# Optimization experiments

Measured on AMD Instinct MI355X. Metric: run time of the kernel, lower is better.

Reference implementation:

```python
import jax, jax.numpy as jnp
import numpy as np

T, H, I, E = 1024, 2048, 3200, 8  # tokens, hidden, intermediate, experts
JITTER_EPS = 0.01


def sparsemixer(scores, jitter_eps=JITTER_EPS):
    # ---- top-1 ----
    max1 = jnp.max(scores, axis=-1, keepdims=True)
    ind1 = jnp.argmax(scores, axis=-1, keepdims=True)  # first-max, matches torch
    factor = jnp.maximum(jnp.abs(scores), max1)        # clamp(min=max1)
    mask = (max1 - scores) / factor > 2.0 * jitter_eps
    masked_gates = jax.nn.softmax(jnp.where(mask, -jnp.inf, scores), axis=-1)
    mult1 = jnp.take_along_axis(masked_gates, ind1, axis=-1)
    # ---- mask out top-1, then top-2 ----
    top1_onehot = jax.nn.one_hot(ind1[..., 0], scores.shape[-1], dtype=bool)
    masked_scores = jnp.where(top1_onehot, -jnp.inf, scores)
    max2 = jnp.max(masked_scores, axis=-1, keepdims=True)
    ind2 = jnp.argmax(masked_scores, axis=-1, keepdims=True)
    factor2 = jnp.maximum(jnp.abs(scores), max2)
    mask2 = (max2 - scores) / factor2 > 2.0 * jitter_eps
    masked_gates2 = jax.nn.softmax(jnp.where(mask2, -jnp.inf, masked_scores), axis=-1)
    mult2 = jnp.take_along_axis(masked_gates2, ind2, axis=-1)
    multiplier = jnp.concatenate([mult1, mult2], axis=-1)       # [T, 2]
    selected = jnp.concatenate([ind1, ind2], axis=-1)           # [T, 2] int
    return multiplier, selected


def setup_inputs() -> dict:
    key = jax.random.key(0)
    k0, k1, k2, k3, k4 = jax.random.split(key, 5)
    hidden_states = jax.random.normal(k0, (T, H), dtype=jnp.float32)
    gate_w = jax.random.normal(k1, (E, H), dtype=jnp.float32) * (H ** -0.5)
    w1 = jax.random.normal(k2, (E, I, H), dtype=jnp.float32) * (H ** -0.5)
    w3 = jax.random.normal(k3, (E, I, H), dtype=jnp.float32) * (H ** -0.5)
    w2 = jax.random.normal(k4, (E, H, I), dtype=jnp.float32) * (I ** -0.5)
    return {"hidden_states": hidden_states, "gate_w": gate_w,
            "w1": w1, "w3": w3, "w2": w2}


def reference(hidden_states, gate_w, w1, w3, w2):
    x = hidden_states.reshape(-1, gate_w.shape[1])              # [T, H]
    router_logits = x @ gate_w.T                                # [T, E]
    topk_w, topk_ids = sparsemixer(router_logits)               # [T,2], [T,2]
    n_exp = gate_w.shape[0]
    # combine top-2 (weight, id) pairs into a dense [T, E] gate matrix
    gates = jnp.sum(jax.nn.one_hot(topk_ids, n_exp, dtype=x.dtype)
                    * topk_w[..., None], axis=1)                # [T, E]
    # SiLU-gated expert MLPs, combined with routing gates
    h1 = jnp.einsum('th,eih->tei', x, w1)                       # [T, E, I]
    h3 = jnp.einsum('th,eih->tei', x, w3)
    act = jax.nn.silu(h1) * h3                                  # [T, E, I]
    out = jnp.einsum('tei,ehi,te->th', act, w2, gates)          # [T, H]
    return out.reshape(hidden_states.shape)
```

## Files before the change

kernel.cpp:

```cpp
#include <hip/hip_runtime.h>

#define T_ 1024
#define H_ 2048
#define I_ 3200
#define E_ 8

typedef float fvec4 __attribute__((ext_vector_type(4)));
typedef float f32x4 __attribute__((ext_vector_type(4)));
typedef __bf16 bf16x8 __attribute__((ext_vector_type(8)));
typedef unsigned short u16x4 __attribute__((ext_vector_type(4)));

typedef const __attribute__((address_space(1))) void* gp1_t;
typedef __attribute__((address_space(3))) void* sp3_t;

#define WS_CHUNK 128
#define WS_TOK   512
#define WS_GATE  33280
#define WS_XB    66560
#define WS_ACT   4261888
#define MAXCH    20

#define BARX() { asm volatile("s_waitcnt lgkmcnt(0)" ::: "memory"); \
    __builtin_amdgcn_sched_barrier(0); __builtin_amdgcn_s_barrier(); \
    __builtin_amdgcn_sched_barrier(0); }

__global__ __launch_bounds__(256) void router_kernel(const float* __restrict__ x,
                                                     const float* __restrict__ gw,
                                                     int* __restrict__ cnt,
                                                     int* __restrict__ tok,
                                                     float* __restrict__ gate,
                                                     unsigned short* __restrict__ xb) {
  const int lane = threadIdx.x & 63;
  const int wv = threadIdx.x >> 6;
  const int t = blockIdx.x * 4 + wv;

  const float* xp = x + (size_t)t * H_;
  fvec4 xr[8];
#pragma unroll
  for (int j = 0; j < 8; ++j) xr[j] = *(const fvec4*)(xp + j * 256 + lane * 4);

  unsigned short* xbp = xb + (size_t)t * H_;
#pragma unroll
  for (int j = 0; j < 8; ++j) {
    u16x4 o;
#pragma unroll
    for (int c = 0; c < 4; ++c) o[c] = __builtin_bit_cast(unsigned short, (__bf16)xr[j][c]);
    *(u16x4*)(xbp + j * 256 + lane * 4) = o;
  }

  float s[E_];
#pragma unroll
  for (int e = 0; e < E_; ++e) {
    const float* gp = gw + (size_t)e * H_;
    float p = 0.f;
#pragma unroll
    for (int j = 0; j < 8; ++j) {
      fvec4 g = *(const fvec4*)(gp + j * 256 + lane * 4);
      p = fmaf(xr[j][0], g[0], p); p = fmaf(xr[j][1], g[1], p);
      p = fmaf(xr[j][2], g[2], p); p = fmaf(xr[j][3], g[3], p);
    }
#pragma unroll
    for (int off = 32; off > 0; off >>= 1) p += __shfl_xor(p, off);
    s[e] = p;
  }

  float max1 = s[0]; int i1 = 0;
#pragma unroll
  for (int e = 1; e < E_; ++e) if (s[e] > max1) { max1 = s[e]; i1 = e; }
  float den1 = 0.f;
#pragma unroll
  for (int e = 0; e < E_; ++e) {
    float factor = fmaxf(fabsf(s[e]), max1);
    if ((max1 - s[e]) <= 0.02f * factor) den1 += expf(s[e] - max1);
  }
  float mult1 = 1.f / den1;

  float max2 = -INFINITY; int i2 = 0;
#pragma unroll
  for (int e = 0; e < E_; ++e) if (e != i1 && s[e] > max2) { max2 = s[e]; i2 = e; }
  float den2 = 0.f;
#pragma unroll
  for (int e = 0; e < E_; ++e) {
    if (e == i1) continue;
    float factor = fmaxf(fabsf(s[e]), max2);
    if ((max2 - s[e]) <= 0.02f * factor) den2 += expf(s[e] - max2);
  }
  float mult2 = 1.f / den2;

  if (lane == 0) {
    int p1 = atomicAdd(&cnt[i1], 1); tok[i1 * T_ + p1] = t; gate[i1 * T_ + p1] = mult1;
    int p2 = atomicAdd(&cnt[i2], 1); tok[i2 * T_ + p2] = t; gate[i2 * T_ + p2] = mult2;
  }
}

__global__ void prefix_kernel(const int* __restrict__ cnt, int* __restrict__ base,
                              int* __restrict__ chunk) {
  if (threadIdx.x == 0 && blockIdx.x == 0) {
    int a = 0, c = 0;
    for (int e = 0; e < E_; ++e) {
      base[e] = a;
      int pc = (cnt[e] + 127) & ~127;
      for (int m = 0; m < pc; m += 256) { chunk[1 + c] = e; chunk[1 + MAXCH + c] = m; ++c; }
      a += pc;
    }
    base[E_] = a;
    chunk[0] = c;
  }
}

__global__ __launch_bounds__(512, 4) void ffn1_kernel(
    const unsigned short* __restrict__ xb, const float* __restrict__ w1,
    const float* __restrict__ w3, const int* __restrict__ cnt,
    const int* __restrict__ base, const int* __restrict__ chunk,
    const int* __restrict__ tokl, unsigned short* __restrict__ actb) {
  if ((int)blockIdx.y >= chunk[0]) return;
  const int e = chunk[1 + blockIdx.y];
  const int m_base = chunk[1 + MAXCH + blockIdx.y];
  const int ab = base[e];
  const int count = cnt[e];
  const int n0 = blockIdx.x * 32;
  const int tid = threadIdx.x;
  const int lane = tid & 63, wv = tid >> 6;
  const int wm = wv >> 1, wn = wv & 1;

  __shared__ unsigned short Ab[2][256 * 64];
  __shared__ unsigned short B1s[2][32 * 64];
  __shared__ unsigned short B3s[2][32 * 64];

  const unsigned short* aSrc[4];
  const int colg = ((lane & 7) ^ ((lane >> 3) & 7)) * 8;
#pragma unroll
  for (int i = 0; i < 4; ++i) {
    int r = m_base + wv * 32 + i * 8 + (lane >> 3);
    if (r >= count) r = count - 1;
    aSrc[i] = xb + (size_t)tokl[e * T_ + r] * H_ + colg;
  }
  const int brow = tid >> 4, w = tid & 15;
  const float* b1p = w1 + ((size_t)e * I_ + n0 + brow) * H_ + w * 4;
  const float* b3p = w3 + ((size_t)e * I_ + n0 + brow) * H_ + w * 4;
  const int wbyte = brow * 128 + (((w >> 1) ^ (brow & 7)) << 4) + (w & 1) * 8;

  f32x4 acc1[4], acc3[4];
#pragma unroll
  for (int mi = 0; mi < 4; ++mi) { acc1[mi] = (f32x4){0,0,0,0}; acc3[mi] = (f32x4){0,0,0,0}; }

  auto STAGE_A = [&](unsigned short* dst, int kb) {
#pragma unroll
    for (int i = 0; i < 4; ++i)
      __builtin_amdgcn_global_load_lds((gp1_t)(aSrc[i] + kb),
                                       (sp3_t)(dst + (wv * 32 + i * 8) * 64), 16, 0, 0);
  };
  auto CVTW = [&](fvec4& r1, fvec4& r3, int buf) {
    u16x4 v, u;
#pragma unroll
    for (int cc = 0; cc < 4; ++cc) {
      v[cc] = __builtin_bit_cast(unsigned short, (__bf16)r1[cc]);
      u[cc] = __builtin_bit_cast(unsigned short, (__bf16)r3[cc]);
    }
    *(u16x4*)((char*)B1s[buf] + wbyte) = v;
    *(u16x4*)((char*)B3s[buf] + wbyte) = u;
  };
  auto STEP = [&](const unsigned short* A_, int bbuf) {
#pragma unroll
    for (int kk = 0; kk < 2; ++kk) {
      const int c16 = kk * 4 + (lane >> 4);
      bf16x8 af[4];
#pragma unroll
      for (int mi = 0; mi < 4; ++mi) {
        int ar = wm * 64 + mi * 16 + (lane & 15);
        af[mi] = *(const bf16x8*)((const char*)A_ + ar * 128 + ((c16 ^ (ar & 7)) << 4));
      }
      int br = wn * 16 + (lane & 15);
      bf16x8 f1 = *(const bf16x8*)((const char*)B1s[bbuf] + br * 128 + ((c16 ^ (br & 7)) << 4));
      bf16x8 f3 = *(const bf16x8*)((const char*)B3s[bbuf] + br * 128 + ((c16 ^ (br & 7)) << 4));
      __builtin_amdgcn_s_setprio(1);
#pragma unroll
      for (int mi = 0; mi < 4; ++mi) {
        acc1[mi] = __builtin_amdgcn_mfma_f32_16x16x32_bf16(af[mi], f1, acc1[mi], 0, 0, 0);
        acc3[mi] = __builtin_amdgcn_mfma_f32_16x16x32_bf16(af[mi], f3, acc3[mi], 0, 0, 0);
      }
      __builtin_amdgcn_s_setprio(0);
    }
  };

  const int NT = H_ / 64;
  fvec4 cv1, cv3;
  fvec4 fl1, fl3;
  fvec4 fr1, fr3;

  STAGE_A(Ab[0], 0);
  fr1 = *(const fvec4*)(b1p);       fr3 = *(const fvec4*)(b3p);
  cv1 = *(const fvec4*)(b1p + 64);  cv3 = *(const fvec4*)(b3p + 64);
  fl1 = *(const fvec4*)(b1p + 128); fl3 = *(const fvec4*)(b3p + 128);
  asm volatile("s_waitcnt vmcnt(2)" ::: "memory");
  CVTW(fr1, fr3, 0);
  BARX();

  for (int t = 0; t < NT; ++t) {
    const int cur = t & 1;
    if (t + 1 < NT) {
      STAGE_A(Ab[cur ^ 1], (t + 1) * 64);
      CVTW(cv1, cv3, cur ^ 1);
    }
    if (t + 3 < NT) {
      fr1 = *(const fvec4*)(b1p + (t + 3) * 64);
      fr3 = *(const fvec4*)(b3p + (t + 3) * 64);
    }
    STEP(Ab[cur], cur);
    if (t + 3 < NT) { asm volatile("s_waitcnt vmcnt(2)" ::: "memory"); }
    else            { asm volatile("s_waitcnt vmcnt(0)" ::: "memory"); }
    BARX();
    fvec4 z1 = cv1, z3 = cv3;
    cv1 = fl1; cv3 = fl3;
    fl1 = fr1; fl3 = fr3;
    fr1 = z1;  fr3 = z3;
  }

  const int row_lim = (base[e + 1] - ab) - m_base;
#pragma unroll
  for (int mi = 0; mi < 4; ++mi)
#pragma unroll
    for (int j = 0; j < 4; ++j) {
      int row = wm * 64 + mi * 16 + (lane >> 4) * 4 + j;
      if (row < row_lim) {
        float h1 = acc1[mi][j];
        float a = (h1 / (1.f + __expf(-h1))) * acc3[mi][j];
        actb[(size_t)(ab + m_base + row) * I_ + n0 + wn * 16 + (lane & 15)] =
            __builtin_bit_cast(unsigned short, (__bf16)a);
      }
    }
}

__global__ __launch_bounds__(512, 4) void ffn2_kernel(
    const unsigned short* __restrict__ actb, const float* __restrict__ w2,
    const int* __restrict__ cnt, const int* __restrict__ base,
    const int* __restrict__ chunk, const int* __restrict__ tokl,
    const float* __restrict__ gatel, float* __restrict__ out) {
  if ((int)blockIdx.y >= chunk[0]) return;
  const int e = chunk[1 + blockIdx.y];
  const int m_base = chunk[1 + MAXCH + blockIdx.y];
  const int count = cnt[e];
  if (m_base >= count) return;
  const int ab = base[e];
  const int n0 = blockIdx.x * 64;
  const int tid = threadIdx.x;
  const int lane = tid & 63, wv = tid >> 6;
  const int wm = wv >> 2, wn = wv & 3;

  __shared__ unsigned short Ab[2][256 * 64];
  __shared__ unsigned short Bs[2][64 * 64];

  const unsigned short* aSrc[4];
  const int colg = ((lane & 7) ^ ((lane >> 3) & 7)) * 8;
#pragma unroll
  for (int i = 0; i < 4; ++i) {
    int r = ab + m_base + wv * 32 + i * 8 + (lane >> 3);
    aSrc[i] = actb + (size_t)r * I_ + colg;
  }
  const int brow = tid >> 3, w = tid & 7;
  const float* bp = w2 + ((size_t)e * H_ + n0 + brow) * I_ + w * 8;
  const int wbyte = brow * 128 + ((w ^ (brow & 7)) << 4);

  f32x4 acc[8];
#pragma unroll
  for (int mi = 0; mi < 8; ++mi) acc[mi] = (f32x4){0,0,0,0};

  auto STAGE_A = [&](unsigned short* dst, int kb) {
#pragma unroll
    for (int i = 0; i < 4; ++i)
      __builtin_amdgcn_global_load_lds((gp1_t)(aSrc[i] + kb),
                                       (sp3_t)(dst + (wv * 32 + i * 8) * 64), 16, 0, 0);
  };
  auto CVTW = [&](fvec4& r0, fvec4& r1, int buf) {
    bf16x8 v;
#pragma unroll
    for (int cc = 0; cc < 4; ++cc) { v[cc] = (__bf16)r0[cc]; v[cc + 4] = (__bf16)r1[cc]; }
    *(bf16x8*)((char*)Bs[buf] + wbyte) = v;
  };
  auto STEP = [&](const unsigned short* A_, int bbuf) {
#pragma unroll
    for (int kk = 0; kk < 2; ++kk) {
      const int c16 = kk * 4 + (lane >> 4);
      int br = wn * 16 + (lane & 15);
      bf16x8 f = *(const bf16x8*)((const char*)Bs[bbuf] + br * 128 + ((c16 ^ (br & 7)) << 4));
      __builtin_amdgcn_s_setprio(1);
#pragma unroll
      for (int mi = 0; mi < 8; ++mi) {
        int ar = wm * 128 + mi * 16 + (lane & 15);
        bf16x8 af = *(const bf16x8*)((const char*)A_ + ar * 128 + ((c16 ^ (ar & 7)) << 4));
        acc[mi] = __builtin_amdgcn_mfma_f32_16x16x32_bf16(af, f, acc[mi], 0, 0, 0);
      }
      __builtin_amdgcn_s_setprio(0);
    }
  };

  const int NT = I_ / 64;
  fvec4 cv0, cv1, fl0, fl1, fr0, fr1;

  STAGE_A(Ab[0], 0);
  fr0 = *(const fvec4*)(bp);       fr1 = *(const fvec4*)(bp + 4);
  cv0 = *(const fvec4*)(bp + 64);  cv1 = *(const fvec4*)(bp + 68);
  fl0 = *(const fvec4*)(bp + 128); fl1 = *(const fvec4*)(bp + 132);
  asm volatile("s_waitcnt vmcnt(2)" ::: "memory");
  CVTW(fr0, fr1, 0);
  BARX();

  for (int t = 0; t < NT; ++t) {
    const int cur = t & 1;
    if (t + 1 < NT) {
      STAGE_A(Ab[cur ^ 1], (t + 1) * 64);
      CVTW(cv0, cv1, cur ^ 1);
    }
    if (t + 3 < NT) {
      fr0 = *(const fvec4*)(bp + (t + 3) * 64);
      fr1 = *(const fvec4*)(bp + (t + 3) * 64 + 4);
    }
    STEP(Ab[cur], cur);
    if (t + 3 < NT) { asm volatile("s_waitcnt vmcnt(2)" ::: "memory"); }
    else            { asm volatile("s_waitcnt vmcnt(0)" ::: "memory"); }
    BARX();
    fvec4 z0 = cv0, z1 = cv1;
    cv0 = fl0; cv1 = fl1;
    fl0 = fr0; fl1 = fr1;
    fr0 = z0;  fr1 = z1;
  }

#pragma unroll
  for (int mi = 0; mi < 8; ++mi)
#pragma unroll
    for (int j = 0; j < 4; ++j) {
      int row = m_base + wm * 128 + mi * 16 + (lane >> 4) * 4 + j;
      if (row < count) {
        int tokv = tokl[e * T_ + row];
        float g = gatel[e * T_ + row];
        atomicAdd(&out[(size_t)tokv * H_ + n0 + wn * 16 + (lane & 15)], g * acc[mi][j]);
      }
    }
}

extern "C" void kernel_launch(void* const* d_in, const int* in_sizes, int n_in,
                              void* d_out, int out_size, void* d_ws, size_t ws_size,
                              hipStream_t stream) {
  const float* x  = (const float*)d_in[0];
  const float* gw = (const float*)d_in[1];
  const float* w1 = (const float*)d_in[2];
  const float* w3 = (const float*)d_in[3];
  const float* w2 = (const float*)d_in[4];
  float* out = (float*)d_out;
  char* ws = (char*)d_ws;

  int* cnt = (int*)ws;
  int* base = (int*)(ws + 64);
  int* chunk = (int*)(ws + WS_CHUNK);
  int* tokl = (int*)(ws + WS_TOK);
  float* gatel = (float*)(ws + WS_GATE);
  unsigned short* xb = (unsigned short*)(ws + WS_XB);
  unsigned short* actb = (unsigned short*)(ws + WS_ACT);

  (void)hipMemsetAsync(d_out, 0, (size_t)T_ * H_ * sizeof(float), stream);
  (void)hipMemsetAsync(ws, 0, 64, stream);

  router_kernel<<<T_ / 4, 256, 0, stream>>>(x, gw, cnt, tokl, gatel, xb);
  prefix_kernel<<<1, 64, 0, stream>>>(cnt, base, chunk);
  ffn1_kernel<<<dim3(I_ / 32, MAXCH), 512, 0, stream>>>(xb, w1, w3, cnt, base, chunk, tokl, actb);
  ffn2_kernel<<<dim3(H_ / 64, MAXCH), 512, 0, stream>>>(actb, w2, cnt, base, chunk, tokl, gatel, out);
}
```

Baseline: 311.6 us.

## Widen expert GEMM N-tiles, split K in down-projection, single-buffer weight LDS

Doubles the N tile in both expert GEMMs: 64 columns in the gate/up kernel and 128 in the down kernel. Each A fragment now feeds two MFMA columns, and the routed activations are re-read fewer times. The down-projection is also split in two along K via a third grid dimension, relying on the existing atomic accumulation to restore parallelism lost to the wider tiles. Weight staging moves to a single LDS buffer fed by two register sets of four float4 loads each, with an extra barrier per iteration. The trade-offs are higher register pressure, more atomics in the down kernel, and more synchronisation per K step.

```diff
diff --git a/kernel.cpp b/kernel.cpp
--- a/kernel.cpp
+++ b/kernel.cpp
@@ -18,8 +18,10 @@
 #define WS_GATE  33280
 #define WS_XB    66560
 #define WS_ACT   4261888
-#define MAXCH    20
-
+#define MAXCH    32
+
+#define BARS() { __builtin_amdgcn_sched_barrier(0); __builtin_amdgcn_s_barrier(); \
+    __builtin_amdgcn_sched_barrier(0); }
 #define BARX() { asm volatile("s_waitcnt lgkmcnt(0)" ::: "memory"); \
     __builtin_amdgcn_sched_barrier(0); __builtin_amdgcn_s_barrier(); \
     __builtin_amdgcn_sched_barrier(0); }
@@ -118,14 +120,14 @@
   const int m_base = chunk[1 + MAXCH + blockIdx.y];
   const int ab = base[e];
   const int count = cnt[e];
-  const int n0 = blockIdx.x * 32;
+  const int n0 = blockIdx.x * 64;
   const int tid = threadIdx.x;
   const int lane = tid & 63, wv = tid >> 6;
   const int wm = wv >> 1, wn = wv & 1;
 
   __shared__ unsigned short Ab[2][256 * 64];
-  __shared__ unsigned short B1s[2][32 * 64];
-  __shared__ unsigned short B3s[2][32 * 64];
+  __shared__ unsigned short B1s[64 * 64];
+  __shared__ unsigned short B3s[64 * 64];
 
   const unsigned short* aSrc[4];
   const int colg = ((lane & 7) ^ ((lane >> 3) & 7)) * 8;
@@ -135,14 +137,19 @@
     if (r >= count) r = count - 1;
     aSrc[i] = xb + (size_t)tokl[e * T_ + r] * H_ + colg;
   }
-  const int brow = tid >> 4, w = tid & 15;
-  const float* b1p = w1 + ((size_t)e * I_ + n0 + brow) * H_ + w * 4;
-  const float* b3p = w3 + ((size_t)e * I_ + n0 + brow) * H_ + w * 4;
-  const int wbyte = brow * 128 + (((w >> 1) ^ (brow & 7)) << 4) + (w & 1) * 8;
-
-  f32x4 acc1[4], acc3[4];
-#pragma unroll
-  for (int mi = 0; mi < 4; ++mi) { acc1[mi] = (f32x4){0,0,0,0}; acc3[mi] = (f32x4){0,0,0,0}; }
+  const int bt = tid & 255;
+  const int brow = bt >> 2;
+  const float* bp = ((wv < 4) ? w1 : w3) + ((size_t)e * I_ + n0 + brow) * H_ + (bt & 3) * 16;
+  unsigned short* Bout = (wv < 4) ? B1s : B3s;
+  const int c0 = (bt & 3) * 2;
+  const int wb0 = brow * 128 + ((c0 ^ (brow & 7)) << 4);
+  const int wb1 = brow * 128 + (((c0 + 1) ^ (brow & 7)) << 4);
+
+  f32x4 acc1[4][2], acc3[4][2];
+#pragma unroll
+  for (int mi = 0; mi < 4; ++mi)
+#pragma unroll
+    for (int ni = 0; ni < 2; ++ni) { acc1[mi][ni] = (f32x4){0,0,0,0}; acc3[mi][ni] = (f32x4){0,0,0,0}; }
 
   auto STAGE_A = [&](unsigned short* dst, int kb) {
 #pragma unroll
@@ -150,85 +157,85 @@
       __builtin_amdgcn_global_load_lds((gp1_t)(aSrc[i] + kb),
                                        (sp3_t)(dst + (wv * 32 + i * 8) * 64), 16, 0, 0);
   };
-  auto CVTW = [&](fvec4& r1, fvec4& r3, int buf) {
-    u16x4 v, u;
+  auto LOADB = [&](fvec4 (&r)[4], int kb) {
+#pragma unroll
+    for (int j = 0; j < 4; ++j) r[j] = *(const fvec4*)(bp + kb + j * 4);
+  };
+  auto CVTW = [&](fvec4 (&r)[4]) {
+    bf16x8 v0, v1;
 #pragma unroll
     for (int cc = 0; cc < 4; ++cc) {
-      v[cc] = __builtin_bit_cast(unsigned short, (__bf16)r1[cc]);
-      u[cc] = __builtin_bit_cast(unsigned short, (__bf16)r3[cc]);
-    }
-    *(u16x4*)((char*)B1s[buf] + wbyte) = v;
-    *(u16x4*)((char*)B3s[buf] + wbyte) = u;
-  };
-  auto STEP = [&](const unsigned short* A_, int bbuf) {
+      v0[cc] = (__bf16)r[0][cc]; v0[cc + 4] = (__bf16)r[1][cc];
+      v1[cc] = (__bf16)r[2][cc]; v1[cc + 4] = (__bf16)r[3][cc];
+    }
+    *(bf16x8*)((char*)Bout + wb0) = v0;
+    *(bf16x8*)((char*)Bout + wb1) = v1;
+  };
+  auto STEP = [&](const unsigned short* A_) {
 #pragma unroll
     for (int kk = 0; kk < 2; ++kk) {
       const int c16 = kk * 4 + (lane >> 4);
-      bf16x8 af[4];
+      bf16x8 af[4], f1[2], f3[2];
 #pragma unroll
       for (int mi = 0; mi < 4; ++mi) {
         int ar = wm * 64 + mi * 16 + (lane & 15);
         af[mi] = *(const bf16x8*)((const char*)A_ + ar * 128 + ((c16 ^ (ar & 7)) << 4));
       }
-      int br = wn * 16 + (lane & 15);
-      bf16x8 f1 = *(const bf16x8*)((const char*)B1s[bbuf] + br * 128 + ((c16 ^ (br & 7)) << 4));
-      bf16x8 f3 = *(const bf16x8*)((const char*)B3s[bbuf] + br * 128 + ((c16 ^ (br & 7)) << 4));
+#pragma unroll
+      for (int ni = 0; ni < 2; ++ni) {
+        int br = wn * 32 + ni * 16 + (lane & 15);
+        f1[ni] = *(const bf16x8*)((const char*)B1s + br * 128 + ((c16 ^ (br & 7)) << 4));
+        f3[ni] = *(const bf16x8*)((const char*)B3s + br * 128 + ((c16 ^ (br & 7)) << 4));
+      }
       __builtin_amdgcn_s_setprio(1);
 #pragma unroll
-      for (int mi = 0; mi < 4; ++mi) {
-        acc1[mi] = __builtin_amdgcn_mfma_f32_16x16x32_bf16(af[mi], f1, acc1[mi], 0, 0, 0);
-        acc3[mi] = __builtin_amdgcn_mfma_f32_16x16x32_bf16(af[mi], f3, acc3[mi], 0, 0, 0);
-      }
+      for (int mi = 0; mi < 4; ++mi)
+#pragma unroll
+        for (int ni = 0; ni < 2; ++ni) {
+          acc1[mi][ni] = __builtin_amdgcn_mfma_f32_16x16x32_bf16(af[mi], f1[ni], acc1[mi][ni], 0, 0, 0);
+          acc3[mi][ni] = __builtin_amdgcn_mfma_f32_16x16x32_bf16(af[mi], f3[ni], acc3[mi][ni], 0, 0, 0);
+        }
       __builtin_amdgcn_s_setprio(0);
     }
   };
 
   const int NT = H_ / 64;
-  fvec4 cv1, cv3;
-  fvec4 fl1, fl3;
-  fvec4 fr1, fr3;
-
+  fvec4 bE[4], bO[4];
+
+  LOADB(bE, 0);
   STAGE_A(Ab[0], 0);
-  fr1 = *(const fvec4*)(b1p);       fr3 = *(const fvec4*)(b3p);
-  cv1 = *(const fvec4*)(b1p + 64);  cv3 = *(const fvec4*)(b3p + 64);
-  fl1 = *(const fvec4*)(b1p + 128); fl3 = *(const fvec4*)(b3p + 128);
-  asm volatile("s_waitcnt vmcnt(2)" ::: "memory");
-  CVTW(fr1, fr3, 0);
+  LOADB(bO, 64);
+  asm volatile("s_waitcnt vmcnt(4)" ::: "memory");
+  CVTW(bE);
   BARX();
 
   for (int t = 0; t < NT; ++t) {
     const int cur = t & 1;
-    if (t + 1 < NT) {
-      STAGE_A(Ab[cur ^ 1], (t + 1) * 64);
-      CVTW(cv1, cv3, cur ^ 1);
-    }
-    if (t + 3 < NT) {
-      fr1 = *(const fvec4*)(b1p + (t + 3) * 64);
-      fr3 = *(const fvec4*)(b3p + (t + 3) * 64);
-    }
-    STEP(Ab[cur], cur);
-    if (t + 3 < NT) { asm volatile("s_waitcnt vmcnt(2)" ::: "memory"); }
+    if (t + 1 < NT) STAGE_A(Ab[cur ^ 1], (t + 1) * 64);
+    if (t + 2 < NT) { if (!cur) LOADB(bE, (t + 2) * 64); else LOADB(bO, (t + 2) * 64); }
+    STEP(Ab[cur]);
+    if (t + 2 < NT) { asm volatile("s_waitcnt vmcnt(4)" ::: "memory"); }
     else            { asm volatile("s_waitcnt vmcnt(0)" ::: "memory"); }
+    BARS();
+    if (t + 1 < NT) { if (!cur) CVTW(bO); else CVTW(bE); }
     BARX();
-    fvec4 z1 = cv1, z3 = cv3;
-    cv1 = fl1; cv3 = fl3;
-    fl1 = fr1; fl3 = fr3;
-    fr1 = z1;  fr3 = z3;
   }
 
   const int row_lim = (base[e + 1] - ab) - m_base;
 #pragma unroll
   for (int mi = 0; mi < 4; ++mi)
 #pragma unroll
-    for (int j = 0; j < 4; ++j) {
-      int row = wm * 64 + mi * 16 + (lane >> 4) * 4 + j;
-      if (row < row_lim) {
-        float h1 = acc1[mi][j];
-        float a = (h1 / (1.f + __expf(-h1))) * acc3[mi][j];
-        actb[(size_t)(ab + m_base + row) * I_ + n0 + wn * 16 + (lane & 15)] =
-            __builtin_bit_cast(unsigned short, (__bf16)a);
-      }
-    }
+    for (int ni = 0; ni < 2; ++ni)
+#pragma unroll
+      for (int j = 0; j < 4; ++j) {
+        int row = wm * 64 + mi * 16 + (lane >> 4) * 4 + j;
+        if (row < row_lim) {
+          float h1 = acc1[mi][ni][j];
+          float a = (h1 / (1.f + __expf(-h1))) * acc3[mi][ni][j];
+          actb[(size_t)(ab + m_base + row) * I_ + n0 + wn * 32 + ni * 16 + (lane & 15)] =
+              __builtin_bit_cast(unsigned short, (__bf16)a);
+        }
+      }
 }
 
 __global__ __launch_bounds__(512, 4) void ffn2_kernel(
@@ -242,28 +249,33 @@
   const int count = cnt[e];
   if (m_base >= count) return;
   const int ab = base[e];
-  const int n0 = blockIdx.x * 64;
+  const int n0 = blockIdx.x * 128;
+  const int k0 = blockIdx.z * 1600;
   const int tid = threadIdx.x;
   const int lane = tid & 63, wv = tid >> 6;
   const int wm = wv >> 2, wn = wv & 3;
 
   __shared__ unsigned short Ab[2][256 * 64];
-  __shared__ unsigned short Bs[2][64 * 64];
+  __shared__ unsigned short Bs[128 * 64];
 
   const unsigned short* aSrc[4];
   const int colg = ((lane & 7) ^ ((lane >> 3) & 7)) * 8;
 #pragma unroll
   for (int i = 0; i < 4; ++i) {
     int r = ab + m_base + wv * 32 + i * 8 + (lane >> 3);
-    aSrc[i] = actb + (size_t)r * I_ + colg;
-  }
-  const int brow = tid >> 3, w = tid & 7;
-  const float* bp = w2 + ((size_t)e * H_ + n0 + brow) * I_ + w * 8;
-  const int wbyte = brow * 128 + ((w ^ (brow & 7)) << 4);
-
-  f32x4 acc[8];
-#pragma unroll
-  for (int mi = 0; mi < 8; ++mi) acc[mi] = (f32x4){0,0,0,0};
+    aSrc[i] = actb + (size_t)r * I_ + k0 + colg;
+  }
+  const int brow = tid >> 2;
+  const float* bp = w2 + ((size_t)e * H_ + n0 + brow) * I_ + k0 + (tid & 3) * 16;
+  const int c0 = (tid & 3) * 2;
+  const int wb0 = brow * 128 + ((c0 ^ (brow & 7)) << 4);
+  const int wb1 = brow * 128 + (((c0 + 1) ^ (brow & 7)) << 4);
+
+  f32x4 acc[8][2];
+#pragma unroll
+  for (int mi = 0; mi < 8; ++mi)
+#pragma unroll
+    for (int ni = 0; ni < 2; ++ni) acc[mi][ni] = (f32x4){0,0,0,0};
 
   auto STAGE_A = [&](unsigned short* dst, int kb) {
 #pragma unroll
@@ -271,58 +283,63 @@
       __builtin_amdgcn_global_load_lds((gp1_t)(aSrc[i] + kb),
                                        (sp3_t)(dst + (wv * 32 + i * 8) * 64), 16, 0, 0);
   };
-  auto CVTW = [&](fvec4& r0, fvec4& r1, int buf) {
-    bf16x8 v;
-#pragma unroll
-    for (int cc = 0; cc < 4; ++cc) { v[cc] = (__bf16)r0[cc]; v[cc + 4] = (__bf16)r1[cc]; }
-    *(bf16x8*)((char*)Bs[buf] + wbyte) = v;
-  };
-  auto STEP = [&](const unsigned short* A_, int bbuf) {
+  auto LOADB = [&](fvec4 (&r)[4], int kb) {
+#pragma unroll
+    for (int j = 0; j < 4; ++j) r[j] = *(const fvec4*)(bp + kb + j * 4);
+  };
+  auto CVTW = [&](fvec4 (&r)[4]) {
+    bf16x8 v0, v1;
+#pragma unroll
+    for (int cc = 0; cc < 4; ++cc) {
+      v0[cc] = (__bf16)r[0][cc]; v0[cc + 4] = (__bf16)r[1][cc];
+      v1[cc] = (__bf16)r[2][cc]; v1[cc + 4] = (__bf16)r[3][cc];
+    }
+    *(bf16x8*)((char*)Bs + wb0) = v0;
+    *(bf16x8*)((char*)Bs + wb1) = v1;
+  };
+  auto STEP = [&](const unsigned short* A_) {
 #pragma unroll
     for (int kk = 0; kk < 2; ++kk) {
       const int c16 = kk * 4 + (lane >> 4);
-      int br = wn * 16 + (lane & 15);
-      bf16x8 f = *(const bf16x8*)((const char*)Bs[bbuf] + br * 128 + ((c16 ^ (br & 7)) << 4));
+      bf16x8 f[2];
+#pragma unroll
+      for (int ni = 0; ni < 2; ++ni) {
+        int br = wn * 32 + ni * 16 + (lane & 15);
+        f[ni] = *(const bf16x8*)((const char*)Bs + br * 128 + ((c16 ^ (br & 7)) << 4));
+      }
       __builtin_amdgcn_s_setprio(1);
 #pragma unroll
       for (int mi = 0; mi < 8; ++mi) {
         int ar = wm * 128 + mi * 16 + (lane & 15);
         bf16x8 af = *(const bf16x8*)((const char*)A_ + ar * 128 + ((c16 ^ (ar & 7)) << 4));
-        acc[mi] = __builtin_amdgcn_mfma_f32_16x16x32_bf16(af, f, acc[mi], 0, 0, 0);
+#pragma unroll
+        for (int ni = 0; ni < 2; ++ni)
+          acc[mi][ni] = __builtin_amdgcn_mfma_f32_16x16x32_bf16(af, f[ni], acc[mi][ni], 0, 0, 0);
       }
       __builtin_amdgcn_s_setprio(0);
     }
   };
 
-  const int NT = I_ / 64;
-  fvec4 cv0, cv1, fl0, fl1, fr0, fr1;
-
+  const int NT = 1600 / 64;
+  fvec4 bE[4], bO[4];
+
+  LOADB(bE, 0);
   STAGE_A(Ab[0], 0);
-  fr0 = *(const fvec4*)(bp);       fr1 = *(const fvec4*)(bp + 4);
-  cv0 = *(const fvec4*)(bp + 64);  cv1 = *(const fvec4*)(bp + 68);
-  fl0 = *(const fvec4*)(bp + 128); fl1 = *(const fvec4*)(bp + 132);
-  asm volatile("s_waitcnt vmcnt(2)" ::: "memory");
-  CVTW(fr0, fr1, 0);
+  LOADB(bO, 64);
+  asm volatile("s_waitcnt vmcnt(4)" ::: "memory");
+  CVTW(bE);
   BARX();
 
   for (int t = 0; t < NT; ++t) {
     const int cur = t & 1;
-    if (t + 1 < NT) {
-      STAGE_A(Ab[cur ^ 1], (t + 1) * 64);
-      CVTW(cv0, cv1, cur ^ 1);
-    }
-    if (t + 3 < NT) {
-      fr0 = *(const fvec4*)(bp + (t + 3) * 64);
-      fr1 = *(const fvec4*)(bp + (t + 3) * 64 + 4);
-    }
-    STEP(Ab[cur], cur);
-    if (t + 3 < NT) { asm volatile("s_waitcnt vmcnt(2)" ::: "memory"); }
+    if (t + 1 < NT) STAGE_A(Ab[cur ^ 1], (t + 1) * 64);
+    if (t + 2 < NT) { if (!cur) LOADB(bE, (t + 2) * 64); else LOADB(bO, (t + 2) * 64); }
+    STEP(Ab[cur]);
+    if (t + 2 < NT) { asm volatile("s_waitcnt vmcnt(4)" ::: "memory"); }
     else            { asm volatile("s_waitcnt vmcnt(0)" ::: "memory"); }
+    BARS();
+    if (t + 1 < NT) { if (!cur) CVTW(bO); else CVTW(bE); }
     BARX();
-    fvec4 z0 = cv0, z1 = cv1;
-    cv0 = fl0; cv1 = fl1;
-    fl0 = fr0; fl1 = fr1;
-    fr0 = z0;  fr1 = z1;
   }
 
 #pragma unroll
@@ -333,7 +350,10 @@
       if (row < count) {
         int tokv = tokl[e * T_ + row];
         float g = gatel[e * T_ + row];
-        atomicAdd(&out[(size_t)tokv * H_ + n0 + wn * 16 + (lane & 15)], g * acc[mi][j]);
+#pragma unroll
+        for (int ni = 0; ni < 2; ++ni)
+          atomicAdd(&out[(size_t)tokv * H_ + n0 + wn * 32 + ni * 16 + (lane & 15)],
+                    g * acc[mi][ni][j]);
       }
     }
 }
@@ -362,6 +382,6 @@
 
   router_kernel<<<T_ / 4, 256, 0, stream>>>(x, gw, cnt, tokl, gatel, xb);
   prefix_kernel<<<1, 64, 0, stream>>>(cnt, base, chunk);
-  ffn1_kernel<<<dim3(I_ / 32, MAXCH), 512, 0, stream>>>(xb, w1, w3, cnt, base, chunk, tokl, actb);
-  ffn2_kernel<<<dim3(H_ / 64, MAXCH), 512, 0, stream>>>(actb, w2, cnt, base, chunk, tokl, gatel, out);
-}
+  ffn1_kernel<<<dim3(I_ / 64, MAXCH), 512, 0, stream>>>(xb, w1, w3, cnt, base, chunk, tokl, actb);
+  ffn2_kernel<<<dim3(H_ / 128, MAXCH, 2), 512, 0, stream>>>(actb, w2, cnt, base, chunk, tokl, gatel, out);
+}
```

Result: slower. 578.9 us (+85.8%).

## Single-buffer A tile in LDS, raise occupancy, split-K ffn2 over two halves

Applied to the files above, without the earlier changes.

Both FFN kernels drop the double-buffered activation tile in LDS for a single buffer. Each iteration now runs the MFMA step first, then a barrier, then issues the next global-to-LDS load. This frees LDS so the launch bound can go from 4 to 6 blocks per CU. ffn2 is also split along the intermediate dimension into two z-blocks, each doing half of K, which doubles the grid and relies on the existing atomicAdd to combine results. The trade-off is that the A-tile load is no longer overlapped with compute, and atomic traffic on the output doubles.

```diff
diff --git a/kernel.cpp b/kernel.cpp
--- a/kernel.cpp
+++ b/kernel.cpp
@@ -20,6 +20,8 @@
 #define WS_ACT   4261888
 #define MAXCH    20
 
+#define BAR1() { __builtin_amdgcn_sched_barrier(0); __builtin_amdgcn_s_barrier(); \
+    __builtin_amdgcn_sched_barrier(0); }
 #define BARX() { asm volatile("s_waitcnt lgkmcnt(0)" ::: "memory"); \
     __builtin_amdgcn_sched_barrier(0); __builtin_amdgcn_s_barrier(); \
     __builtin_amdgcn_sched_barrier(0); }
@@ -108,7 +110,7 @@
   }
 }
 
-__global__ __launch_bounds__(512, 4) void ffn1_kernel(
+__global__ __launch_bounds__(512, 6) void ffn1_kernel(
     const unsigned short* __restrict__ xb, const float* __restrict__ w1,
     const float* __restrict__ w3, const int* __restrict__ cnt,
     const int* __restrict__ base, const int* __restrict__ chunk,
@@ -123,7 +125,7 @@
   const int lane = tid & 63, wv = tid >> 6;
   const int wm = wv >> 1, wn = wv & 1;
 
-  __shared__ unsigned short Ab[2][256 * 64];
+  __shared__ unsigned short Ab[256 * 64];
   __shared__ unsigned short B1s[2][32 * 64];
   __shared__ unsigned short B3s[2][32 * 64];
 
@@ -144,11 +146,11 @@
 #pragma unroll
   for (int mi = 0; mi < 4; ++mi) { acc1[mi] = (f32x4){0,0,0,0}; acc3[mi] = (f32x4){0,0,0,0}; }
 
-  auto STAGE_A = [&](unsigned short* dst, int kb) {
+  auto STAGE_A = [&](int kb) {
 #pragma unroll
     for (int i = 0; i < 4; ++i)
       __builtin_amdgcn_global_load_lds((gp1_t)(aSrc[i] + kb),
-                                       (sp3_t)(dst + (wv * 32 + i * 8) * 64), 16, 0, 0);
+                                       (sp3_t)(Ab + (wv * 32 + i * 8) * 64), 16, 0, 0);
   };
   auto CVTW = [&](fvec4& r1, fvec4& r3, int buf) {
     u16x4 v, u;
@@ -160,7 +162,7 @@
     *(u16x4*)((char*)B1s[buf] + wbyte) = v;
     *(u16x4*)((char*)B3s[buf] + wbyte) = u;
   };
-  auto STEP = [&](const unsigned short* A_, int bbuf) {
+  auto STEP = [&](int bbuf) {
 #pragma unroll
     for (int kk = 0; kk < 2; ++kk) {
       const int c16 = kk * 4 + (lane >> 4);
@@ -168,7 +170,7 @@
 #pragma unroll
       for (int mi = 0; mi < 4; ++mi) {
         int ar = wm * 64 + mi * 16 + (lane & 15);
-        af[mi] = *(const bf16x8*)((const char*)A_ + ar * 128 + ((c16 ^ (ar & 7)) << 4));
+        af[mi] = *(const bf16x8*)((const char*)Ab + ar * 128 + ((c16 ^ (ar & 7)) << 4));
       }
       int br = wn * 16 + (lane & 15);
       bf16x8 f1 = *(const bf16x8*)((const char*)B1s[bbuf] + br * 128 + ((c16 ^ (br & 7)) << 4));
@@ -188,27 +190,30 @@
   fvec4 fl1, fl3;
   fvec4 fr1, fr3;
 
-  STAGE_A(Ab[0], 0);
+  STAGE_A(0);
+  __builtin_amdgcn_sched_barrier(0);
   fr1 = *(const fvec4*)(b1p);       fr3 = *(const fvec4*)(b3p);
   cv1 = *(const fvec4*)(b1p + 64);  cv3 = *(const fvec4*)(b3p + 64);
   fl1 = *(const fvec4*)(b1p + 128); fl3 = *(const fvec4*)(b3p + 128);
-  asm volatile("s_waitcnt vmcnt(2)" ::: "memory");
+  asm volatile("s_waitcnt vmcnt(4)" ::: "memory");
   CVTW(fr1, fr3, 0);
   BARX();
 
   for (int t = 0; t < NT; ++t) {
     const int cur = t & 1;
-    if (t + 1 < NT) {
-      STAGE_A(Ab[cur ^ 1], (t + 1) * 64);
-      CVTW(cv1, cv3, cur ^ 1);
-    }
+    STEP(cur);
+    if (t + 1 == NT) break;
+    BAR1();
+    STAGE_A((t + 1) * 64);
+    __builtin_amdgcn_sched_barrier(0);
+    CVTW(cv1, cv3, cur ^ 1);
     if (t + 3 < NT) {
       fr1 = *(const fvec4*)(b1p + (t + 3) * 64);
       fr3 = *(const fvec4*)(b3p + (t + 3) * 64);
-    }
-    STEP(Ab[cur], cur);
-    if (t + 3 < NT) { asm volatile("s_waitcnt vmcnt(2)" ::: "memory"); }
-    else            { asm volatile("s_waitcnt vmcnt(0)" ::: "memory"); }
+      asm volatile("s_waitcnt vmcnt(2)" ::: "memory");
+    } else {
+      asm volatile("s_waitcnt vmcnt(0)" ::: "memory");
+    }
     BARX();
     fvec4 z1 = cv1, z3 = cv3;
     cv1 = fl1; cv3 = fl3;
@@ -231,7 +236,7 @@
     }
 }
 
-__global__ __launch_bounds__(512, 4) void ffn2_kernel(
+__global__ __launch_bounds__(512, 6) void ffn2_kernel(
     const unsigned short* __restrict__ actb, const float* __restrict__ w2,
     const int* __restrict__ cnt, const int* __restrict__ base,
     const int* __restrict__ chunk, const int* __restrict__ tokl,
@@ -243,11 +248,12 @@
   if (m_base >= count) return;
   const int ab = base[e];
   const int n0 = blockIdx.x * 64;
+  const int k0 = blockIdx.z * (I_ / 2);
   const int tid = threadIdx.x;
   const int lane = tid & 63, wv = tid >> 6;
   const int wm = wv >> 2, wn = wv & 3;
 
-  __shared__ unsigned short Ab[2][256 * 64];
+  __shared__ unsigned short Ab[256 * 64];
   __shared__ unsigned short Bs[2][64 * 64];
 
   const unsigned short* aSrc[4];
@@ -255,21 +261,21 @@
 #pragma unroll
   for (int i = 0; i < 4; ++i) {
     int r = ab + m_base + wv * 32 + i * 8 + (lane >> 3);
-    aSrc[i] = actb + (size_t)r * I_ + colg;
+    aSrc[i] = actb + (size_t)r * I_ + k0 + colg;
   }
   const int brow = tid >> 3, w = tid & 7;
-  const float* bp = w2 + ((size_t)e * H_ + n0 + brow) * I_ + w * 8;
+  const float* bp = w2 + ((size_t)e * H_ + n0 + brow) * I_ + k0 + w * 8;
   const int wbyte = brow * 128 + ((w ^ (brow & 7)) << 4);
 
   f32x4 acc[8];
 #pragma unroll
   for (int mi = 0; mi < 8; ++mi) acc[mi] = (f32x4){0,0,0,0};
 
-  auto STAGE_A = [&](unsigned short* dst, int kb) {
+  auto STAGE_A = [&](int kb) {
 #pragma unroll
     for (int i = 0; i < 4; ++i)
       __builtin_amdgcn_global_load_lds((gp1_t)(aSrc[i] + kb),
-                                       (sp3_t)(dst + (wv * 32 + i * 8) * 64), 16, 0, 0);
+                                       (sp3_t)(Ab + (wv * 32 + i * 8) * 64), 16, 0, 0);
   };
   auto CVTW = [&](fvec4& r0, fvec4& r1, int buf) {
     bf16x8 v;
@@ -277,7 +283,7 @@
     for (int cc = 0; cc < 4; ++cc) { v[cc] = (__bf16)r0[cc]; v[cc + 4] = (__bf16)r1[cc]; }
     *(bf16x8*)((char*)Bs[buf] + wbyte) = v;
   };
-  auto STEP = [&](const unsigned short* A_, int bbuf) {
+  auto STEP = [&](int bbuf) {
 #pragma unroll
     for (int kk = 0; kk < 2; ++kk) {
       const int c16 = kk * 4 + (lane >> 4);
@@ -287,37 +293,40 @@
 #pragma unroll
       for (int mi = 0; mi < 8; ++mi) {
         int ar = wm * 128 + mi * 16 + (lane & 15);
-        bf16x8 af = *(const bf16x8*)((const char*)A_ + ar * 128 + ((c16 ^ (ar & 7)) << 4));
+        bf16x8 af = *(const bf16x8*)((const char*)Ab + ar * 128 + ((c16 ^ (ar & 7)) << 4));
         acc[mi] = __builtin_amdgcn_mfma_f32_16x16x32_bf16(af, f, acc[mi], 0, 0, 0);
       }
       __builtin_amdgcn_s_setprio(0);
     }
   };
 
-  const int NT = I_ / 64;
+  const int NT = (I_ / 2) / 64;
   fvec4 cv0, cv1, fl0, fl1, fr0, fr1;
 
-  STAGE_A(Ab[0], 0);
+  STAGE_A(0);
+  __builtin_amdgcn_sched_barrier(0);
   fr0 = *(const fvec4*)(bp);       fr1 = *(const fvec4*)(bp + 4);
   cv0 = *(const fvec4*)(bp + 64);  cv1 = *(const fvec4*)(bp + 68);
   fl0 = *(const fvec4*)(bp + 128); fl1 = *(const fvec4*)(bp + 132);
-  asm volatile("s_waitcnt vmcnt(2)" ::: "memory");
+  asm volatile("s_waitcnt vmcnt(4)" ::: "memory");
   CVTW(fr0, fr1, 0);
   BARX();
 
   for (int t = 0; t < NT; ++t) {
     const int cur = t & 1;
-    if (t + 1 < NT) {
-      STAGE_A(Ab[cur ^ 1], (t + 1) * 64);
-      CVTW(cv0, cv1, cur ^ 1);
-    }
+    STEP(cur);
+    if (t + 1 == NT) break;
+    BAR1();
+    STAGE_A((t + 1) * 64);
+    __builtin_amdgcn_sched_barrier(0);
+    CVTW(cv0, cv1, cur ^ 1);
     if (t + 3 < NT) {
       fr0 = *(const fvec4*)(bp + (t + 3) * 64);
       fr1 = *(const fvec4*)(bp + (t + 3) * 64 + 4);
-    }
-    STEP(Ab[cur], cur);
-    if (t + 3 < NT) { asm volatile("s_waitcnt vmcnt(2)" ::: "memory"); }
-    else            { asm volatile("s_waitcnt vmcnt(0)" ::: "memory"); }
+      asm volatile("s_waitcnt vmcnt(2)" ::: "memory");
+    } else {
+      asm volatile("s_waitcnt vmcnt(0)" ::: "memory");
+    }
     BARX();
     fvec4 z0 = cv0, z1 = cv1;
     cv0 = fl0; cv1 = fl1;
@@ -363,5 +372,5 @@
   router_kernel<<<T_ / 4, 256, 0, stream>>>(x, gw, cnt, tokl, gatel, xb);
   prefix_kernel<<<1, 64, 0, stream>>>(cnt, base, chunk);
   ffn1_kernel<<<dim3(I_ / 32, MAXCH), 512, 0, stream>>>(xb, w1, w3, cnt, base, chunk, tokl, actb);
-  ffn2_kernel<<<dim3(H_ / 64, MAXCH), 512, 0, stream>>>(actb, w2, cnt, base, chunk, tokl, gatel, out);
-}
+  ffn2_kernel<<<dim3(H_ / 64, MAXCH, 2), 512, 0, stream>>>(actb, w2, cnt, base, chunk, tokl, gatel, out);
+}
```

After: 1.031 ms. 231% more time.
